# Kernel optimization log

Hardware: AMD Instinct MI355X
Metric: run time of the kernel (lower is better)

## Reference

```python
import jax, jax.numpy as jnp
import numpy as np

# Module config (mirrors init_kwargs)
B = 131072          # batch of trajectories
N_STATES = 16       # n_x_f + n_x_b
N_SEL = 8           # states selected per subnet (band width of Binary_mat)
N_U = 4             # inputs
N_FEAT = 64         # hidden width, neuron_list = [64, 64]
N_OUT = 16          # n_x_o, one output per subnet

# Binary_mat[i, j] = 1 iff (j - i) mod 16 < 8. The torch loop collects selected
# indices in INCREASING j order, so sort each row's selected set.
IDX = np.sort((np.arange(N_OUT)[:, None] + np.arange(N_SEL)[None, :]) % N_STATES, axis=1)  # [16, 8] int


def setup_inputs() -> dict:
    key = jax.random.key(0)
    k0, k1, k2, k3, k4, k5 = jax.random.split(key, 6)
    zin = N_SEL + N_U  # 12 = per-subnet MLP input width
    return {
        "x_f": jax.random.normal(k0, (B, 8), jnp.float32),
        "x_b": jax.random.normal(k1, (B, 8), jnp.float32),
        "u": jax.random.normal(k2, (B, N_U), jnp.float32),
        # stacked per-subnet weights (nn.Linear stores [out, in]); no biases
        "W0": jax.random.normal(k3, (N_OUT, N_FEAT, zin), jnp.float32) * 0.05,
        "W1": jax.random.normal(k4, (N_OUT, N_FEAT, N_FEAT), jnp.float32) * 0.05,
        "W2": jax.random.normal(k5, (N_OUT, 1, N_FEAT), jnp.float32) * 0.05,
    }


def reference(x_f, x_b, u, W0, W1, W2):
    # x_tilde = cat(x_f, x_b): [B, 16]
    x_tilde = jnp.concatenate([x_f, x_b], axis=-1)
    # Per-subnet gather of its selected state subset: [B, 16(sub), 8]
    x_sel = x_tilde[:, IDX]
    # Append exogenous input u to every subnet's input: [B, 16, 12]
    u_b = jnp.broadcast_to(u[:, None, :], (u.shape[0], N_OUT, N_U))
    z = jnp.concatenate([x_sel, u_b], axis=-1)
    # Grouped small MLPs (Linear+Tanh, Linear+Tanh, Linear) as batched GEMMs
    h = jnp.tanh(jnp.einsum('bsi,soi->bso', z, W0))   # [B, 16, 64]
    h = jnp.tanh(jnp.einsum('bsh,soh->bso', h, W1))   # [B, 16, 64]
    dx = jnp.einsum('bsh,soh->bso', h, W2)[..., 0]    # scatter into dx slices -> [B, 16]
    return dx
```

## Files before the change

kernel.cpp:

```cpp
#include <hip/hip_runtime.h>


#define N_STATES 16
#define CHUNK    4

typedef _Float16 f16x8  __attribute__((ext_vector_type(8)));
typedef float    f32x16 __attribute__((ext_vector_type(16)));
typedef __fp16   h2     __attribute__((ext_vector_type(2)));
typedef unsigned int u32x2 __attribute__((ext_vector_type(2)));

__device__ __forceinline__ h2 pack2(float a, float b) {
    return __builtin_amdgcn_cvt_pkrtz(a, b);
}
__device__ __forceinline__ unsigned int h2_bits(h2 v) {
    union { h2 h; unsigned int u; } x; x.h = v; return x.u;
}
__device__ __forceinline__ h2 bits_h2(unsigned int v) {
    union { unsigned int u; h2 h; } x; x.u = v; return x.h;
}
__device__ __forceinline__ f16x8 u4_to_h8(uint4 v) {
    union { uint4 u; f16x8 h; } x; x.u = v; return x.h;
}
__device__ __forceinline__ uint4 pk8(float4 a, float4 b) {
    return make_uint4(h2_bits(pack2(a.x, a.y)), h2_bits(pack2(a.z, a.w)),
                      h2_bits(pack2(b.x, b.y)), h2_bits(pack2(b.z, b.w)));
}

__device__ __forceinline__ h2 tanh_pk(h2 x) {
    const h2 hi = {(__fp16)1.25f, (__fp16)1.25f};
    const h2 lo = {(__fp16)-1.25f, (__fp16)-1.25f};
    x = __builtin_elementwise_min(__builtin_elementwise_max(x, lo), hi);
    h2 s = x * x;
    const h2 c4 = {(__fp16)0.00598591f, (__fp16)0.00598591f};
    const h2 c3 = {(__fp16)-0.03807894f, (__fp16)-0.03807894f};
    const h2 c2 = {(__fp16)0.12576901f, (__fp16)0.12576901f};
    const h2 c1 = {(__fp16)-0.33203310f, (__fp16)-0.33203310f};
    const h2 c0 = {(__fp16)0.99998110f, (__fp16)0.99998110f};
    h2 p = s * c4 + c3;
    p = s * p + c2;
    p = s * p + c1;
    p = s * p + c0;
    return x * p;
}

__global__ __launch_bounds__(256, 5) void fans_mfma_kernel(
    const float* __restrict__ x_f, const float* __restrict__ x_b,
    const float* __restrict__ u,   const float* __restrict__ W0,
    const float* __restrict__ W1,  const float* __restrict__ W2,
    float* __restrict__ out)
{
    __shared__ __align__(16) uint4 zplA[256];
    __shared__ __align__(16) uint2 zplB[256];
    __shared__ __align__(16) uint4 sA1[8][64];
    __shared__ __align__(16) uint4 sA0[2][64];
    __shared__ __align__(16) unsigned int w2l[32];

    const int s   = blockIdx.y;
    const int tid = threadIdx.x;
    const int b0  = blockIdx.x * (256 * CHUNK);

    const int lid = tid & 63;
    const int w   = tid >> 6;
    const int n   = lid & 31;
    const int h   = lid >> 5;

    {
        const int r  = tid >> 2;
        const int kc = tid & 3;
        const float* p = W1 + s * 4096 + r * 64 + kc * 16;
        const float4 v0 = ((const float4*)p)[0];
        const float4 v1 = ((const float4*)p)[1];
        const float4 v2 = ((const float4*)p)[2];
        const float4 v3 = ((const float4*)p)[3];
        sA1[(r >> 5) * 4 + kc][(r & 31)]      = pk8(v0, v1);
        sA1[(r >> 5) * 4 + kc][32 + (r & 31)] = pk8(v2, v3);
    }
    if (tid < 128) {
        const int r  = tid >> 1;
        const int hh = tid & 1;
        const float* base = W0 + s * 768 + r * 12;
        uint4 v;
        if (hh == 0) {
            const float4 v0 = *(const float4*)(base + 0);
            const float4 v1 = *(const float4*)(base + 4);
            v = pk8(v0, v1);
        } else {
            const float4 v0 = *(const float4*)(base + 8);
            v = make_uint4(h2_bits(pack2(v0.x, v0.y)), h2_bits(pack2(v0.z, v0.w)), 0u, 0u);
        }
        sA0[r >> 5][hh * 32 + (r & 31)] = v;
    }
    if (tid < 32) {
        const float* w2s = W2 + s * 64;
        w2l[tid] = h2_bits(pack2(w2s[2 * tid], w2s[2 * tid + 1]));
    }
    __syncthreads();

    const int wrap = (s > 8) ? (s - 8) : 0;

    #pragma unroll 1
    for (int ch = 0; ch < CHUNK; ++ch) {
        const int rbase = b0 + ch * 256;

        {
            const int row = rbase + tid;
            float zs[8];
            #pragma unroll
            for (int j = 0; j < 8; ++j) {
                const int idx = (j < wrap) ? j : (s + j - wrap);
                zs[j] = (idx < 8) ? x_f[row * 8 + idx] : x_b[row * 8 + (idx - 8)];
            }
            const float4 uv = *(const float4*)(u + row * 4);
            zplA[tid] = make_uint4(h2_bits(pack2(zs[0], zs[1])), h2_bits(pack2(zs[2], zs[3])),
                                   h2_bits(pack2(zs[4], zs[5])), h2_bits(pack2(zs[6], zs[7])));
            zplB[tid] = make_uint2(h2_bits(pack2(uv.x, uv.y)), h2_bits(pack2(uv.z, uv.w)));
        }

        #pragma unroll
        for (int m = 0; m < 2; ++m) {
            const int rowb = 64 * w + 32 * m;

            unsigned int zero = 0;
            asm("" : "+v"(zero));
            const int lz = lid + (int)zero;

            f16x8 zf;
            if (h == 0) {
                zf = u4_to_h8(zplA[rowb + n]);
            } else {
                const uint2 b = zplB[rowb + n];
                zf = u4_to_h8(make_uint4(b.x, b.y, 0u, 0u));
            }

            const f32x16 z16 = {0.f,0.f,0.f,0.f,0.f,0.f,0.f,0.f,
                                0.f,0.f,0.f,0.f,0.f,0.f,0.f,0.f};
            const f16x8 a0a = u4_to_h8(sA0[0][lz]);
            const f16x8 a0b = u4_to_h8(sA0[1][lz]);
            f32x16 c1a = __builtin_amdgcn_mfma_f32_32x32x16_f16(a0a, zf, z16, 0, 0, 0);
            f32x16 c1b = __builtin_amdgcn_mfma_f32_32x32x16_f16(a0b, zf, z16, 0, 0, 0);

            unsigned int pw[16];
            #pragma unroll
            for (int a = 0; a < 4; ++a) {
                const int r = 4 * a;
                pw[2 * a + 0]     = h2_bits(tanh_pk(pack2(c1a[r],     c1a[r + 1])));
                pw[2 * a + 1]     = h2_bits(tanh_pk(pack2(c1a[r + 2], c1a[r + 3])));
                pw[8 + 2 * a + 0] = h2_bits(tanh_pk(pack2(c1b[r],     c1b[r + 1])));
                pw[8 + 2 * a + 1] = h2_bits(tanh_pk(pack2(c1b[r + 2], c1b[r + 3])));
            }

            f32x16 c2a = z16, c2b = z16;
            #pragma unroll
            for (int kc = 0; kc < 4; ++kc) {
                const int q = 8 * (kc >> 1) + 4 * (kc & 1);
                u32x2 r0 = __builtin_amdgcn_permlane32_swap(pw[q + 0], pw[q + 2], false, false);
                u32x2 r1 = __builtin_amdgcn_permlane32_swap(pw[q + 1], pw[q + 3], false, false);
                const f16x8 hb  = u4_to_h8(make_uint4(r0.x, r1.x, r0.y, r1.y));
                const f16x8 w1a = u4_to_h8(sA1[kc][lz]);
                const f16x8 w1b = u4_to_h8(sA1[4 + kc][lz]);
                c2a = __builtin_amdgcn_mfma_f32_32x32x16_f16(w1a, hb, c2a, 0, 0, 0);
                c2b = __builtin_amdgcn_mfma_f32_32x32x16_f16(w1b, hb, c2b, 0, 0, 0);
            }

            const unsigned int* w2z = &w2l[zero];
            float p0 = 0.f, p1 = 0.f, q0 = 0.f, q1 = 0.f;
            #pragma unroll
            for (int a = 0; a < 4; ++a) {
                const int r = 4 * a;
                const uint2 wa = *(const uint2*)&w2z[4 * a + 2 * h];
                const uint2 wb = *(const uint2*)&w2z[16 + 4 * a + 2 * h];
                if (a & 1) {
                    p1 = __builtin_amdgcn_fdot2(tanh_pk(pack2(c2a[r], c2a[r + 1])), bits_h2(wa.x), p1, false);
                    p1 = __builtin_amdgcn_fdot2(tanh_pk(pack2(c2a[r + 2], c2a[r + 3])), bits_h2(wa.y), p1, false);
                    q1 = __builtin_amdgcn_fdot2(tanh_pk(pack2(c2b[r], c2b[r + 1])), bits_h2(wb.x), q1, false);
                    q1 = __builtin_amdgcn_fdot2(tanh_pk(pack2(c2b[r + 2], c2b[r + 3])), bits_h2(wb.y), q1, false);
                } else {
                    p0 = __builtin_amdgcn_fdot2(tanh_pk(pack2(c2a[r], c2a[r + 1])), bits_h2(wa.x), p0, false);
                    p0 = __builtin_amdgcn_fdot2(tanh_pk(pack2(c2a[r + 2], c2a[r + 3])), bits_h2(wa.y), p0, false);
                    q0 = __builtin_amdgcn_fdot2(tanh_pk(pack2(c2b[r], c2b[r + 1])), bits_h2(wb.x), q0, false);
                    q0 = __builtin_amdgcn_fdot2(tanh_pk(pack2(c2b[r + 2], c2b[r + 3])), bits_h2(wb.y), q0, false);
                }
            }
            float acc = (p0 + p1) + (q0 + q1);
            acc += __shfl_xor(acc, 32);

            if (lid < 32)
                out[(rbase + rowb + n) * N_STATES + s] = acc;
        }
    }
}

extern "C" void kernel_launch(void* const* d_in, const int* in_sizes, int n_in,
                              void* d_out, int out_size, void* d_ws, size_t ws_size,
                              hipStream_t stream) {
    const float* x_f = (const float*)d_in[0];
    const float* x_b = (const float*)d_in[1];
    const float* u   = (const float*)d_in[2];
    const float* W0  = (const float*)d_in[3];
    const float* W1  = (const float*)d_in[4];
    const float* W2  = (const float*)d_in[5];
    float* out = (float*)d_out;

    const int nb = in_sizes[0] / 8;
    dim3 grid(nb / (256 * CHUNK), N_STATES);
    fans_mfma_kernel<<<grid, 256, 0, stream>>>(x_f, x_b, u, W0, W1, W2, out);
}
```

Baseline: 121.2 us.

## Remap blocks so each XCD handles all subnets of a batch chunk

Flattens the 2D grid to 1D and remaps the block index so that the 16 subnet blocks sharing one batch chunk land on the same XCD (round-robin dispatch by bid&7). Adjacent subnets then reuse the same x_f/x_b/u rows from that XCD's L2 instead of each XCD fetching them separately. It also interleaves the layer-1 tanh with the layer-2 MFMA loop to shorten live ranges, and raises the launch-bounds occupancy hint from 5 to 6 waves. The higher occupancy target may force register spills.

```diff
diff --git a/kernel.cpp b/kernel.cpp
--- a/kernel.cpp
+++ b/kernel.cpp
@@ -43,7 +43,7 @@
     return x * p;
 }
 
-__global__ __launch_bounds__(256, 5) void fans_mfma_kernel(
+__global__ __launch_bounds__(256, 6) void fans_mfma_kernel(
     const float* __restrict__ x_f, const float* __restrict__ x_b,
     const float* __restrict__ u,   const float* __restrict__ W0,
     const float* __restrict__ W1,  const float* __restrict__ W2,
@@ -55,9 +55,13 @@
     __shared__ __align__(16) uint4 sA0[2][64];
     __shared__ __align__(16) unsigned int w2l[32];
 
-    const int s   = blockIdx.y;
+    const int bid = blockIdx.x;
+    const int xcd = bid & 7;
+    const int t   = bid >> 3;
+    const int s   = t & 15;
+    const int g   = (t >> 4) * 8 + xcd;
     const int tid = threadIdx.x;
-    const int b0  = blockIdx.x * (256 * CHUNK);
+    const int b0  = g * (256 * CHUNK);
 
     const int lid = tid & 63;
     const int w   = tid >> 6;
@@ -139,22 +143,17 @@
             f32x16 c1a = __builtin_amdgcn_mfma_f32_32x32x16_f16(a0a, zf, z16, 0, 0, 0);
             f32x16 c1b = __builtin_amdgcn_mfma_f32_32x32x16_f16(a0b, zf, z16, 0, 0, 0);
 
-            unsigned int pw[16];
-            #pragma unroll
-            for (int a = 0; a < 4; ++a) {
-                const int r = 4 * a;
-                pw[2 * a + 0]     = h2_bits(tanh_pk(pack2(c1a[r],     c1a[r + 1])));
-                pw[2 * a + 1]     = h2_bits(tanh_pk(pack2(c1a[r + 2], c1a[r + 3])));
-                pw[8 + 2 * a + 0] = h2_bits(tanh_pk(pack2(c1b[r],     c1b[r + 1])));
-                pw[8 + 2 * a + 1] = h2_bits(tanh_pk(pack2(c1b[r + 2], c1b[r + 3])));
-            }
-
             f32x16 c2a = z16, c2b = z16;
             #pragma unroll
             for (int kc = 0; kc < 4; ++kc) {
-                const int q = 8 * (kc >> 1) + 4 * (kc & 1);
-                u32x2 r0 = __builtin_amdgcn_permlane32_swap(pw[q + 0], pw[q + 2], false, false);
-                u32x2 r1 = __builtin_amdgcn_permlane32_swap(pw[q + 1], pw[q + 3], false, false);
+                const f32x16 c1s = (kc < 2) ? c1a : c1b;
+                const int r = (kc & 1) * 8;
+                const unsigned int t0 = h2_bits(tanh_pk(pack2(c1s[r],     c1s[r + 1])));
+                const unsigned int t1 = h2_bits(tanh_pk(pack2(c1s[r + 2], c1s[r + 3])));
+                const unsigned int t2 = h2_bits(tanh_pk(pack2(c1s[r + 4], c1s[r + 5])));
+                const unsigned int t3 = h2_bits(tanh_pk(pack2(c1s[r + 6], c1s[r + 7])));
+                u32x2 r0 = __builtin_amdgcn_permlane32_swap(t0, t2, false, false);
+                u32x2 r1 = __builtin_amdgcn_permlane32_swap(t1, t3, false, false);
                 const f16x8 hb  = u4_to_h8(make_uint4(r0.x, r1.x, r0.y, r1.y));
                 const f16x8 w1a = u4_to_h8(sA1[kc][lz]);
                 const f16x8 w1b = u4_to_h8(sA1[4 + kc][lz]);
@@ -202,6 +201,6 @@
     float* out = (float*)d_out;
 
     const int nb = in_sizes[0] / 8;
-    dim3 grid(nb / (256 * CHUNK), N_STATES);
-    fans_mfma_kernel<<<grid, 256, 0, stream>>>(x_f, x_b, u, W0, W1, W2, out);
-}
+    const int nblk = (nb / (256 * CHUNK)) * N_STATES;
+    fans_mfma_kernel<<<dim3(nblk), 256, 0, stream>>>(x_f, x_b, u, W0, W1, W2, out);
+}
```

New measurement: 130.5 us. 7.7% more time.
